# Kernel optimization log

Measured on AMD Instinct MI355X. Metric: run time of the kernel, lower is better.

The kernel has to match this reference:

```python
import jax, jax.numpy as jnp
import numpy as np
from jax import lax

FMAP = 64          # feature map H=W
STRIDE = 16
TILE = 16
IMG = 1024         # image H=W (image_shape[1]==image_shape[2])
PRE_NMS = 1000
POST_NMS = 300
NMS_THR = 0.7
RATIOS = np.array([0.5, 1.0, 2.0])
SCALES = np.array([8.0, 16.0, 32.0])


def _make_anchors():
    # meshgrid order (x, y, ratio, scale) with 'ij' indexing, then reshape(-1, 4)
    gx, gy, gr, gs = np.meshgrid(np.arange(FMAP), np.arange(FMAP),
                                 np.arange(len(RATIOS)), np.arange(len(SCALES)),
                                 indexing='ij')
    half_w = 0.5 * TILE * SCALES[gs] * np.sqrt(RATIOS[gr])
    half_h = 0.5 * TILE * SCALES[gs] * np.sqrt(1.0 / RATIOS[gr])
    cx = (gx + 0.5) * STRIDE
    cy = (gy + 0.5) * STRIDE
    z = np.stack([cx - half_w, cy - half_h, cx + half_w, cy + half_h], axis=-1)
    return jnp.asarray(z.reshape(-1, 4).astype(np.float32))  # (H*W*A, 4)


def setup_inputs() -> dict:
    key = jax.random.key(0)
    ks = jax.random.split(key, 6)
    B, Cin, F, A = 8, 256, 256, 9
    inputs = jax.random.normal(ks[0], (B, Cin, FMAP, FMAP), jnp.float32)
    bboxes = jax.random.uniform(ks[1], (B, 16, 4), jnp.float32) * IMG  # unused in inference path
    w_conv = jax.random.normal(ks[2], (F, Cin, 3, 3), jnp.float32) * 0.02
    b_conv = jnp.zeros((F,), jnp.float32)
    w_clf = jax.random.normal(ks[3], (2 * A, F, 1, 1), jnp.float32) * 0.02
    b_clf = jnp.zeros((2 * A,), jnp.float32)
    w_reg = jax.random.normal(ks[4], (4 * A, F, 1, 1), jnp.float32) * 0.02
    b_reg = jnp.zeros((4 * A,), jnp.float32)
    anchors = _make_anchors()
    return {"inputs": inputs, "bboxes": bboxes, "anchors": anchors,
            "w_conv": w_conv, "b_conv": b_conv,
            "w_clf": w_clf, "b_clf": b_clf,
            "w_reg": w_reg, "b_reg": b_reg}


def _conv(x, w, b):
    y = lax.conv_general_dilated(x, w, (1, 1), 'SAME',
                                 dimension_numbers=('NCHW', 'OIHW', 'NCHW'))
    return y + b[None, :, None, None]


def _nms_rois(boxes, batch_idx):
    # boxes: (PRE_NMS, 4), sorted by score descending. Greedy NMS.
    n = boxes.shape[0]
    lb = jnp.maximum(boxes[:, None, :2], boxes[None, :, :2])
    ub = jnp.minimum(boxes[:, None, 2:], boxes[None, :, 2:])
    inter = jnp.prod(jnp.clip(ub - lb, 0.0), axis=-1)              # (n, n)
    area = jnp.prod(boxes[:, 2:] - boxes[:, :2], axis=-1)          # (n,)
    iou = inter / (area[:, None] + area[None, :] - inter)
    idxs = jnp.arange(n)

    def body(i, keep):
        sup = (iou[i] > NMS_THR) & keep[i] & (idxs > i)
        return keep & ~sup

    keep = lax.fori_loop(0, n, body, jnp.ones((n,), bool))
    # compact kept boxes (in score order) into the first slots; OOB scatter drops
    pos = jnp.where(keep, jnp.cumsum(keep) - 1, n + POST_NMS)
    rois = jnp.zeros((POST_NMS, 5), boxes.dtype).at[:, 0].set(batch_idx.astype(boxes.dtype))
    rois = rois.at[pos, 1:].set(boxes, mode='drop')
    return rois


def reference(inputs, bboxes, anchors, w_conv, b_conv, w_clf, b_clf, w_reg, b_reg):
    B, _, H, W = inputs.shape
    x = jax.nn.relu(_conv(inputs, w_conv, b_conv))                  # (B, F, H, W)
    clf = _conv(x, w_clf, b_clf)                                    # (B, 2A, H, W)
    A = clf.shape[1] // 2
    prob = jax.nn.softmax(clf.reshape(B, 2, A, H, W), axis=1)
    scores = prob[:, 1].transpose(0, 2, 3, 1).reshape(B, -1)        # (B, H*W*A)
    reg = _conv(x, w_reg, b_reg).transpose(0, 2, 3, 1).reshape(B, -1, 4)
    # decode anchors with deltas
    sizes = anchors[:, 2:] - anchors[:, :2]                          # (N, 2)
    centers = 0.5 * (anchors[:, 2:] + anchors[:, :2])
    pred_centers = reg[..., :2] * sizes + centers
    pred_sizes = jnp.exp(reg[..., 2:]) * sizes
    props = jnp.concatenate([pred_centers - 0.5 * pred_sizes,
                             pred_centers + 0.5 * pred_sizes], axis=-1)
    lim = jnp.asarray([IMG - 1, IMG - 1, IMG - 1, IMG - 1], props.dtype)
    props = jnp.clip(props, 0.0, lim)
    # pre-NMS top-k by score
    _, top_idx = lax.top_k(scores, PRE_NMS)
    top_props = jnp.take_along_axis(props, top_idx[..., None], axis=1)  # (B, PRE, 4)
    rois = jax.vmap(_nms_rois)(top_props, jnp.arange(B))            # (B, POST, 5)
    return rois
```

## Files before the change

### kernel.cpp

```cpp
#include <hip/hip_runtime.h>

typedef unsigned long long ULL;
typedef double v4d __attribute__((ext_vector_type(4)));


__device__ __forceinline__ ULL fkey64(double f) {
    ULL u = (ULL)__double_as_longlong(f);
    return (u & 0x8000000000000000ull) ? ~u : (u | 0x8000000000000000ull);
}

__global__ void prep_all(const float* __restrict__ wconv,
                         const float* __restrict__ wclf, const float* __restrict__ bclf,
                         double* __restrict__ wmf,
                         double* __restrict__ wdiff, double* __restrict__ bdiff) {
    int blk = blockIdx.x;
    if (blk < 2304) {
        int e = blk * 256 + threadIdx.x;
        int co = e & 63;
        int r = e >> 6;
        int cil = r & 3;
        int r2 = r >> 2;
        int tap = r2 % 9;
        int r3 = r2 / 9;
        int cg = r3 & 3;
        int cc = r3 >> 2;
        int ci = cc * 4 + cil;
        int gco = cg * 64 + co;
        wmf[e] = (double)wconv[(gco * 256 + ci) * 9 + tap];
    } else {
        int a = blk - 2304;
        int c = threadIdx.x;
        wdiff[a * 256 + c] = (double)wclf[(9 + a) * 256 + c] - (double)wclf[a * 256 + c];
        if (c == 0) bdiff[a] = (double)bclf[9 + a] - (double)bclf[a];
    }
}

__global__ __launch_bounds__(256)
__attribute__((amdgpu_waves_per_eu(4, 4)))
void conv3x3_mfma_f64(
    const float* __restrict__ xin, const double* __restrict__ wmf,
    const float* __restrict__ bias, double* __restrict__ y)
{
    __shared__ double wlds[2304];
    __shared__ float  xs[1152];

    const int t = threadIdx.x;
    const int blk = blockIdx.x;
    const int b = blk >> 7;
    const int rp = (blk >> 2) & 31;
    const int cg = blk & 3;
    const int h0 = rp * 2;
    const int lane = t & 63;
    const int wid = t >> 6;
    const int arow = lane & 15;
    const int kq = lane >> 4;

    int x_ld[5], x_go[5];
#pragma unroll
    for (int i = 0; i < 5; i++) {
        int e = t + i * 256;
        x_ld[i] = -1; x_go[i] = -1;
        if (e < 1056) {
            int cil = e / 264; int rem = e - cil * 264;
            int row = rem / 66; int c = rem - row * 66;
            int hh = h0 - 1 + row; int col = c - 1;
            x_ld[i] = cil * 288 + row * 72 + c;
            if (hh >= 0 && hh < 64 && col >= 0 && col < 64)
                x_go[i] = cil * 4096 + hh * 64 + col;
        }
    }

    const float* xb = xin + (size_t)b * 1048576;
    const double* wsrc = wmf + (size_t)cg * 2304;

    v4d pz = {0.0, 0.0, 0.0, 0.0};
    v4d prow = __builtin_amdgcn_mfma_f64_16x16x4f64((double)arow, 1.0, pz, 0, 0, 0);
    v4d pcol = __builtin_amdgcn_mfma_f64_16x16x4f64(1.0, (double)arow, pz, 0, 0, 0);
    int rmap[4], cmap[4];
#pragma unroll
    for (int g = 0; g < 4; g++) {
        rmap[g] = (int)(prow[g] * 0.25 + 0.5);
        cmap[g] = (int)(pcol[g] * 0.25 + 0.5);
    }

    float xreg[5];
    double wreg[9];
#pragma unroll
    for (int i = 0; i < 5; i++)
        xreg[i] = (x_ld[i] >= 0 && x_go[i] >= 0) ? xb[x_go[i]] : 0.f;
#pragma unroll
    for (int i = 0; i < 9; i++) wreg[i] = wsrc[t + i * 256];

    v4d acc0[4], acc1[4];
#pragma unroll
    for (int nt = 0; nt < 4; nt++) {
        acc0[nt] = (v4d){0.0, 0.0, 0.0, 0.0};
        acc1[nt] = (v4d){0.0, 0.0, 0.0, 0.0};
    }

    for (int cc = 0; cc < 64; ++cc) {
        __syncthreads();
#pragma unroll
        for (int i = 0; i < 5; i++) if (x_ld[i] >= 0) xs[x_ld[i]] = xreg[i];
#pragma unroll
        for (int i = 0; i < 9; i++) wlds[t + i * 256] = wreg[i];
        __syncthreads();

        if (cc < 63) {
#pragma unroll
            for (int i = 0; i < 5; i++)
                xreg[i] = (x_ld[i] >= 0 && x_go[i] >= 0) ? xb[(cc + 1) * 16384 + x_go[i]] : 0.f;
#pragma unroll
            for (int i = 0; i < 9; i++) wreg[i] = wsrc[(size_t)(cc + 1) * 9216 + t + i * 256];
        }

        const float* xsp = xs + kq * 288 + wid * 16 + arow;
        const double* wsp = wlds + kq * 64 + arow;
#pragma unroll
        for (int kh = 0; kh < 3; kh++) {
#pragma unroll
            for (int kw = 0; kw < 3; kw++) {
                const int tap = kh * 3 + kw;
                double a0 = (double)xsp[kh * 72 + kw];
                double a1 = (double)xsp[(kh + 1) * 72 + kw];
#pragma unroll
                for (int nt = 0; nt < 4; nt++) {
                    double bf = wsp[tap * 256 + nt * 16];
                    acc0[nt] = __builtin_amdgcn_mfma_f64_16x16x4f64(a0, bf, acc0[nt], 0, 0, 0);
                    acc1[nt] = __builtin_amdgcn_mfma_f64_16x16x4f64(a1, bf, acc1[nt], 0, 0, 0);
                }
            }
        }
    }

    const size_t pix0 = (size_t)(b * 4096 + h0 * 64 + wid * 16);
#pragma unroll
    for (int nt = 0; nt < 4; nt++) {
#pragma unroll
        for (int g = 0; g < 4; g++) {
            int co = cg * 64 + nt * 16 + cmap[g];
            double bv = (double)bias[co];
            y[(pix0 + rmap[g]) * 256 + co]      = fmax(acc0[nt][g] + bv, 0.0);
            y[(pix0 + 64 + rmap[g]) * 256 + co] = fmax(acc1[nt][g] + bv, 0.0);
        }
    }
}

__global__ __launch_bounds__(256) void head_clf2w(
    const double* __restrict__ y, const double* __restrict__ wdiff,
    const double* __restrict__ bdiff, double* __restrict__ dlog)
{
    const int px = blockIdx.x * 4 + (threadIdx.x >> 6);
    const int lane = threadIdx.x & 63;

    const double* yr = y + (size_t)px * 256;
    double yv[4];
#pragma unroll
    for (int k = 0; k < 4; k++) yv[k] = yr[lane + k * 64];

    double s[9];
#pragma unroll
    for (int a = 0; a < 9; a++) {
        const double* wr = wdiff + a * 256;
        double v = 0.0;
#pragma unroll
        for (int k = 0; k < 4; k++) v = fma(wr[lane + k * 64], yv[k], v);
        s[a] = v;
    }
#pragma unroll
    for (int off = 32; off > 0; off >>= 1) {
#pragma unroll
        for (int a = 0; a < 9; a++) s[a] += __shfl_xor(s[a], off);
    }
    if (lane < 9) dlog[(size_t)px * 9 + lane] = s[lane] + bdiff[lane];
}

__global__ __launch_bounds__(1024, 1) void topk1000(
    const double* __restrict__ dlog, int* __restrict__ selidx)
{
    const int b = blockIdx.x;
    const int t = threadIdx.x;
    const double* d = dlog + (size_t)b * 36864;

    ULL key[36];
#pragma unroll
    for (int j = 0; j < 36; j++) key[j] = fkey64(d[t + j * 1024]);

    __shared__ unsigned int hist[2048];
    __shared__ ULL sh_prefix;
    __shared__ unsigned int sh_need;
    const int rep = (t >> 6) & 7;

    ULL prefix = 0ull;
    int need = 1000;
    for (int rs = 56; rs >= 0; rs -= 8) {
        hist[t] = 0u; hist[t + 1024] = 0u;
        __syncthreads();
        ULL mhi = (rs == 56) ? 0ull : (~0ull << (rs + 8));
#pragma unroll
        for (int j = 0; j < 36; j++) {
            ULL u = key[j];
            if ((u & mhi) == prefix)
                atomicAdd(&hist[rep * 256 + ((unsigned int)(u >> rs) & 255u)], 1u);
        }
        __syncthreads();
        if (t < 64) {
            unsigned int c[4];
#pragma unroll
            for (int j = 0; j < 4; j++) {
                unsigned int s = 0u;
#pragma unroll
                for (int rr = 0; rr < 8; rr++) s += hist[rr * 256 + 4 * t + j];
                c[j] = s;
            }
            const unsigned int s4 = c[0] + c[1] + c[2] + c[3];
            unsigned int S = s4;
#pragma unroll
            for (int off = 1; off < 64; off <<= 1) {
                unsigned int o = __shfl_down(S, off);
                if (t + off < 64) S += o;
            }
            ULL m = __ballot(S >= (unsigned int)need);
            int lstar = 63 - __builtin_clzll(m);
            if (t == lstar) {
                const unsigned int T = S - s4;
                const unsigned int nd = (unsigned int)need;
                int vs; unsigned int ca;
                if (T + c[3] >= nd)                    { vs = 4 * t + 3; ca = T; }
                else if (T + c[3] + c[2] >= nd)        { vs = 4 * t + 2; ca = T + c[3]; }
                else if (T + c[3] + c[2] + c[1] >= nd) { vs = 4 * t + 1; ca = T + c[3] + c[2]; }
                else                    { vs = 4 * t;     ca = T + c[3] + c[2] + c[1]; }
                sh_prefix = prefix | ((ULL)vs << rs);
                sh_need = nd - ca;
            }
        }
        __syncthreads();
        prefix = sh_prefix;
        need = (int)sh_need;
    }

    const ULL K = prefix;
    const int count_above = 1000 - need;
    __shared__ ULL skey[1024];
    __shared__ int sidx[1024];
    __shared__ unsigned int cgt, ceq;
    if (t == 0) { cgt = 0u; ceq = 0u; }
    skey[t] = ~0ull;
    sidx[t] = 0x7FFFFFFF;
    __syncthreads();
#pragma unroll
    for (int j = 0; j < 36; j++) {
        ULL u = key[j];
        int i = t + j * 1024;
        if (u > K) {
            unsigned int s = atomicAdd(&cgt, 1u);
            skey[s] = ~u; sidx[s] = i;
        } else if (u == K) {
            unsigned int s = atomicAdd(&ceq, 1u) + (unsigned int)count_above;
            if (s < 1024u) { skey[s] = ~u; sidx[s] = i; }
        }
    }
    __syncthreads();
    for (int k = 2; k <= 1024; k <<= 1) {
        for (int j = k >> 1; j > 0; j >>= 1) {
            int ixj = t ^ j;
            if (ixj > t) {
                ULL ka = skey[t], kb = skey[ixj];
                int ia = sidx[t], ib = sidx[ixj];
                bool up = ((t & k) == 0);
                bool gt = (ka > kb) || (ka == kb && ia > ib);
                bool lt = (ka < kb) || (ka == kb && ia < ib);
                if (up ? gt : lt) {
                    skey[t] = kb; skey[ixj] = ka;
                    sidx[t] = ib; sidx[ixj] = ia;
                }
            }
            __syncthreads();
        }
    }
    if (t < 1000) selidx[b * 1000 + t] = sidx[t];
}

__global__ __launch_bounds__(256) void decode_boxes2(
    const double* __restrict__ y, const int* __restrict__ selidx,
    const float* __restrict__ wregp, const float* __restrict__ bregp,
    const float* __restrict__ anchors, double4* __restrict__ boxes)
{
    const int roi  = (blockIdx.x * 256 + threadIdx.x) >> 6;
    const int lane = threadIdx.x & 63;
    const int b = roi / 1000;
    const int n = selidx[roi];
    const int a = n % 9;
    const int pix = n / 9;

    const double2* yrow = (const double2*)(y + ((size_t)(b * 4096 + pix)) * 256);
    double2 ya = yrow[lane];
    double2 yc = yrow[lane + 64];

    double s[4];
#pragma unroll
    for (int c = 0; c < 4; c++) {
        const float* wp = wregp + (4 * a + c) * 256;
        float2 wa = *(const float2*)(wp + 2 * lane);
        float2 wc = *(const float2*)(wp + 128 + 2 * lane);
        double v = 0.0;
        v = fma((double)wa.x, ya.x, v);
        v = fma((double)wa.y, ya.y, v);
        v = fma((double)wc.x, yc.x, v);
        v = fma((double)wc.y, yc.y, v);
        s[c] = v;
    }
#pragma unroll
    for (int off = 32; off > 0; off >>= 1) {
#pragma unroll
        for (int c = 0; c < 4; c++) s[c] += __shfl_xor(s[c], off);
    }

    if (lane == 0) {
        double a0 = s[0] + (double)bregp[4 * a + 0];
        double a1 = s[1] + (double)bregp[4 * a + 1];
        double a2 = s[2] + (double)bregp[4 * a + 2];
        double a3 = s[3] + (double)bregp[4 * a + 3];
        float4 an = ((const float4*)anchors)[n];
        double ax1 = an.x, ay1 = an.y, ax2 = an.z, ay2 = an.w;
        double aw = ax2 - ax1, ah = ay2 - ay1;
        double cx = 0.5 * (ax1 + ax2), cy = 0.5 * (ay1 + ay2);
        double pcx = a0 * aw + cx, pcy = a1 * ah + cy;
        double pw = exp(a2) * aw, ph = exp(a3) * ah;
        double x1b = pcx - 0.5 * pw, y1b = pcy - 0.5 * ph;
        double x2b = pcx + 0.5 * pw, y2b = pcy + 0.5 * ph;
        x1b = fmin(fmax(x1b, 0.0), 1023.0);
        y1b = fmin(fmax(y1b, 0.0), 1023.0);
        x2b = fmin(fmax(x2b, 0.0), 1023.0);
        y2b = fmin(fmax(y2b, 0.0), 1023.0);
        double4 o; o.x = x1b; o.y = y1b; o.z = x2b; o.w = y2b;
        boxes[roi] = o;
    }
}

__global__ __launch_bounds__(1024) void nms_mask_k(
    const double4* __restrict__ boxes, ULL* __restrict__ mask)
{
    int b = blockIdx.x >> 3;
    int sub = blockIdx.x & 7;
    __shared__ double4 bx[1000];
    for (int i = threadIdx.x; i < 1000; i += 1024) bx[i] = boxes[b * 1000 + i];
    __syncthreads();
    for (int ml = threadIdx.x; ml < 2000; ml += 1024) {
        int m = sub * 2000 + ml;
        int i = m >> 4;
        int wc = m & 15;
        ULL bits = 0ull;
        int j0 = wc << 6;
        if (j0 + 63 > i) {
            double4 bi = bx[i];
            double ai = (bi.z - bi.x) * (bi.w - bi.y);
            int js = max(j0, i + 1);
            int je = min(j0 + 64, 1000);
            for (int j = js; j < je; j++) {
                double4 bj = bx[j];
                double lx = fmax(bi.x, bj.x), ly = fmax(bi.y, bj.y);
                double ux = fmin(bi.z, bj.z), uy = fmin(bi.w, bj.w);
                double iw = fmax(ux - lx, 0.0), ih = fmax(uy - ly, 0.0);
                double inter = iw * ih;
                double aj = (bj.z - bj.x) * (bj.w - bj.y);
                double iou = inter / (ai + aj - inter);
                if (iou > 0.7) bits |= (1ull << (j - j0));
            }
        }
        mask[(size_t)b * 16000 + m] = bits;
    }
}

__global__ __launch_bounds__(1024) void nms_scan_k(
    const ULL* __restrict__ mask, const double4* __restrict__ boxes,
    float* __restrict__ out)
{
    int b = blockIdx.x;
    int t = threadIdx.x;
    __shared__ ULL smask[16000];
    __shared__ ULL keepw[16];
    {
        const ULL* mrow = mask + (size_t)b * 16000;
        for (int i = t; i < 16000; i += 1024) smask[i] = mrow[i];
    }
    __syncthreads();
    if (t < 64) {
        int lane = t;
        ULL remv = 0ull, cur = 0ull;
        ULL pf[16];
#pragma unroll
        for (int q = 0; q < 16; q++) pf[q] = (lane < 16) ? smask[q * 16 + lane] : 0ull;
        for (int base = 0; base < 1000; base += 16) {
#pragma unroll
            for (int q = 0; q < 16; q++) {
                int i = base + q;
                if (i < 1000) {
                    ULL m = pf[q];
                    int c = i >> 6;
                    ULL mc = __shfl(m, c);
                    bool rem = ((cur >> (i & 63)) & 1ull) != 0ull;
                    if (!rem) { remv |= m; cur |= mc; }
                    if (((i + 1) & 63) == 0) cur = __shfl(remv, (i + 1) >> 6);
                    int nx = i + 16;
                    pf[q] = (lane < 16 && nx < 1000) ? smask[nx * 16 + lane] : 0ull;
                }
            }
        }
        if (lane < 16) keepw[lane] = ~remv;
    }
    __syncthreads();
    if (t < 300) {
        float* row = out + (size_t)(b * 300 + t) * 5;
        row[0] = (float)b; row[1] = 0.f; row[2] = 0.f; row[3] = 0.f; row[4] = 0.f;
    }
    __syncthreads();
    if (t < 1000) {
        ULL kw = keepw[t >> 6];
        if ((kw >> (t & 63)) & 1ull) {
            int pos = (int)__popcll(kw & ((1ull << (t & 63)) - 1ull));
            for (int w = 0; w < (t >> 6); w++) pos += (int)__popcll(keepw[w]);
            if (pos < 300) {
                double4 bv = boxes[b * 1000 + t];
                float* row = out + (size_t)(b * 300 + pos) * 5;
                row[1] = (float)bv.x; row[2] = (float)bv.y;
                row[3] = (float)bv.z; row[4] = (float)bv.w;
            }
        }
    }
}

extern "C" void kernel_launch(void* const* d_in, const int* in_sizes, int n_in,
                              void* d_out, int out_size, void* d_ws, size_t ws_size,
                              hipStream_t stream)
{
    const float* xin     = (const float*)d_in[0];
    const float* anchors = (const float*)d_in[2];
    const float* wconv   = (const float*)d_in[3];
    const float* bconv   = (const float*)d_in[4];
    const float* wclf    = (const float*)d_in[5];
    const float* bclf    = (const float*)d_in[6];
    const float* wregp   = (const float*)d_in[7];
    const float* bregp   = (const float*)d_in[8];
    float* out = (float*)d_out;

    char* base = (char*)d_ws;
    double*  y      = (double*)(base);
    double*  wmf    = (double*)(base + 67108864);
    double4* boxes  = (double4*)(base + 67108864);
    ULL*     mask   = (ULL*)(base + 67364864);
    int*     selidx = (int*)(base + 68388864);
    double*  dlog   = (double*)(base + 71827456);
    double*  wdiff  = (double*)(base + 74186752);
    double*  bdiff  = (double*)(base + 74205184);

    prep_all<<<2313, 256, 0, stream>>>(wconv, wclf, bclf, wmf, wdiff, bdiff);
    conv3x3_mfma_f64<<<1024, 256, 0, stream>>>(xin, wmf, bconv, y);
    head_clf2w<<<8192, 256, 0, stream>>>(y, wdiff, bdiff, dlog);
    topk1000<<<8, 1024, 0, stream>>>(dlog, selidx);
    decode_boxes2<<<2000, 256, 0, stream>>>(y, selidx, wregp, bregp, anchors, boxes);
    nms_mask_k<<<64, 1024, 0, stream>>>(boxes, mask);
    nms_scan_k<<<8, 1024, 0, stream>>>(mask, boxes, out);
}
```

Measured before the change: 936.7 us.

## Drop LDS staging in conv3x3 MFMA kernel, load operands directly from global

Result: slower. 1.004 ms (+7.2%).

```diff
diff --git a/kernel.cpp b/kernel.cpp
--- a/kernel.cpp
+++ b/kernel.cpp
@@ -41,9 +41,6 @@
     const float* __restrict__ xin, const double* __restrict__ wmf,
     const float* __restrict__ bias, double* __restrict__ y)
 {
-    __shared__ double wlds[2304];
-    __shared__ float  xs[1152];
-
     const int t = threadIdx.x;
     const int blk = blockIdx.x;
     const int b = blk >> 7;
@@ -54,24 +51,27 @@
     const int wid = t >> 6;
     const int arow = lane & 15;
     const int kq = lane >> 4;
-
-    int x_ld[5], x_go[5];
-#pragma unroll
-    for (int i = 0; i < 5; i++) {
-        int e = t + i * 256;
-        x_ld[i] = -1; x_go[i] = -1;
-        if (e < 1056) {
-            int cil = e / 264; int rem = e - cil * 264;
-            int row = rem / 66; int c = rem - row * 66;
-            int hh = h0 - 1 + row; int col = c - 1;
-            x_ld[i] = cil * 288 + row * 72 + c;
-            if (hh >= 0 && hh < 64 && col >= 0 && col < 64)
-                x_go[i] = cil * 4096 + hh * 64 + col;
-        }
-    }
-
-    const float* xb = xin + (size_t)b * 1048576;
-    const double* wsrc = wmf + (size_t)cg * 2304;
+    const int col = wid * 16 + arow;
+
+    int roff[4]; float rv[4];
+#pragma unroll
+    for (int r = 0; r < 4; r++) {
+        int hh = h0 - 1 + r;
+        rv[r] = (hh >= 0 && hh < 64) ? 1.f : 0.f;
+        int hc = hh < 0 ? 0 : (hh > 63 ? 63 : hh);
+        roff[r] = hc * 64;
+    }
+    int coff[3]; float cv[3];
+#pragma unroll
+    for (int dc = 0; dc < 3; dc++) {
+        int ic = col + dc - 1;
+        cv[dc] = (ic >= 0 && ic < 64) ? 1.f : 0.f;
+        int cl = ic < 0 ? 0 : (ic > 63 ? 63 : ic);
+        coff[dc] = cl;
+    }
+
+    const float* xq = xin + (size_t)b * 1048576 + kq * 4096;
+    const double* wq = wmf + (size_t)cg * 2304 + kq * 64 + arow;
 
     v4d pz = {0.0, 0.0, 0.0, 0.0};
     v4d prow = __builtin_amdgcn_mfma_f64_16x16x4f64((double)arow, 1.0, pz, 0, 0, 0);
@@ -83,14 +83,6 @@
         cmap[g] = (int)(pcol[g] * 0.25 + 0.5);
     }
 
-    float xreg[5];
-    double wreg[9];
-#pragma unroll
-    for (int i = 0; i < 5; i++)
-        xreg[i] = (x_ld[i] >= 0 && x_go[i] >= 0) ? xb[x_go[i]] : 0.f;
-#pragma unroll
-    for (int i = 0; i < 9; i++) wreg[i] = wsrc[t + i * 256];
-
     v4d acc0[4], acc1[4];
 #pragma unroll
     for (int nt = 0; nt < 4; nt++) {
@@ -99,38 +91,30 @@
     }
 
     for (int cc = 0; cc < 64; ++cc) {
-        __syncthreads();
-#pragma unroll
-        for (int i = 0; i < 5; i++) if (x_ld[i] >= 0) xs[x_ld[i]] = xreg[i];
-#pragma unroll
-        for (int i = 0; i < 9; i++) wlds[t + i * 256] = wreg[i];
-        __syncthreads();
-
-        if (cc < 63) {
-#pragma unroll
-            for (int i = 0; i < 5; i++)
-                xreg[i] = (x_ld[i] >= 0 && x_go[i] >= 0) ? xb[(cc + 1) * 16384 + x_go[i]] : 0.f;
-#pragma unroll
-            for (int i = 0; i < 9; i++) wreg[i] = wsrc[(size_t)(cc + 1) * 9216 + t + i * 256];
-        }
-
-        const float* xsp = xs + kq * 288 + wid * 16 + arow;
-        const double* wsp = wlds + kq * 64 + arow;
+        float xv[4][3];
+#pragma unroll
+        for (int r = 0; r < 4; r++)
+#pragma unroll
+            for (int dc = 0; dc < 3; dc++)
+                xv[r][dc] = xq[roff[r] + coff[dc]] * (rv[r] * cv[dc]);
+
 #pragma unroll
         for (int kh = 0; kh < 3; kh++) {
 #pragma unroll
             for (int kw = 0; kw < 3; kw++) {
                 const int tap = kh * 3 + kw;
-                double a0 = (double)xsp[kh * 72 + kw];
-                double a1 = (double)xsp[(kh + 1) * 72 + kw];
+                double a0 = (double)xv[kh][kw];
+                double a1 = (double)xv[kh + 1][kw];
 #pragma unroll
                 for (int nt = 0; nt < 4; nt++) {
-                    double bf = wsp[tap * 256 + nt * 16];
+                    double bf = wq[tap * 256 + nt * 16];
                     acc0[nt] = __builtin_amdgcn_mfma_f64_16x16x4f64(a0, bf, acc0[nt], 0, 0, 0);
                     acc1[nt] = __builtin_amdgcn_mfma_f64_16x16x4f64(a1, bf, acc1[nt], 0, 0, 0);
                 }
             }
         }
+        xq += 16384;
+        wq += 9216;
     }
 
     const size_t pix0 = (size_t)(b * 4096 + h0 * 64 + wid * 16);
```
